# Kernel optimization log

Measured on AMD Instinct MI355X. Metric: run time of the kernel, lower is better.

## Reference

```python
import jax, jax.numpy as jnp
import numpy as np

N = 14           # num_wires
DEPTH = 2        # feature_map_depth; circuit applies DEPTH+1 StronglyEntanglingLayers blocks
SEL_LAYERS = 2   # params (B, 2*N*3) -> weights (B, 2, N, 3)


def _apply_1q(psi, U, w):
    # psi: (B, 2**N) complex64, U: (B,2,2) complex64, acts on wire w (wire 0 = MSB)
    B = psi.shape[0]
    psi = psi.reshape(B, 2 ** w, 2, -1)
    psi = jnp.einsum('bij,bajc->baic', U, psi)
    return psi.reshape(B, -1)


def _apply_cnot(psi, c, t):
    B = psi.shape[0]
    x = psi.reshape((B,) + (2,) * N)
    ca, ta = 1 + c, 1 + t
    a0 = jax.lax.index_in_dim(x, 0, ca, keepdims=True)
    a1 = jnp.flip(jax.lax.index_in_dim(x, 1, ca, keepdims=True), axis=ta)
    return jnp.concatenate([a0, a1], axis=ca).reshape(B, -1)


def _expz(psi, w):
    # <Z_w> = P(bit_w = 0) - P(bit_w = 1)
    B = psi.shape[0]
    p = (psi.real ** 2 + psi.imag ** 2).reshape(B, 2 ** w, 2, -1)
    return p[:, :, 0].sum(axis=(1, 2)) - p[:, :, 1].sum(axis=(1, 2))


def _rot(phi, theta, omega):
    # PennyLane Rot = RZ(omega) RY(theta) RZ(phi); returns (B,2,2) complex
    c, s = jnp.cos(theta / 2), jnp.sin(theta / 2)
    u00 = jnp.exp(-0.5j * (phi + omega)) * c
    u01 = -jnp.exp(0.5j * (phi - omega)) * s
    u10 = jnp.exp(-0.5j * (phi - omega)) * s
    u11 = jnp.exp(0.5j * (phi + omega)) * c
    return jnp.stack([jnp.stack([u00, u01], -1), jnp.stack([u10, u11], -1)], -2)


def _circuit(phases, weights):
    # phases: (B, N) float32, weights: (B, SEL_LAYERS, N, 3) float32
    B = phases.shape[0]
    psi = jnp.zeros((B, 2 ** N), jnp.complex64).at[:, 0].set(1.0)
    # AngleEmbedding (rotation='X'): RX(phi_w) on each wire
    for w in range(N):
        th = phases[:, w] / 2
        c, s = jnp.cos(th), jnp.sin(th)
        U = jnp.stack([jnp.stack([c + 0j, -1j * s], -1),
                       jnp.stack([-1j * s, c + 0j], -1)], -2)
        psi = _apply_1q(psi, U.astype(jnp.complex64), w)
    # (feature_map_depth + 1) StronglyEntanglingLayers blocks, all sharing `weights`
    for _ in range(DEPTH + 1):
        for l in range(SEL_LAYERS):
            for w in range(N):
                U = _rot(weights[:, l, w, 0], weights[:, l, w, 1], weights[:, l, w, 2])
                psi = _apply_1q(psi, U.astype(jnp.complex64), w)
            r = (l % (N - 1)) + 1  # PennyLane default ranges
            for w in range(N):
                psi = _apply_cnot(psi, w, (w + r) % N)
    return jnp.stack([_expz(psi, w) for w in range(N)], axis=1)  # (B, N)


def setup_inputs() -> dict:
    key = jax.random.key(0)
    k1, k2, k3, k4 = jax.random.split(key, 4)
    B = 512
    return {
        'state_batch': jax.random.normal(k1, (B, 2 ** N, 2), jnp.float32),
        'params': jax.random.normal(k2, (B, SEL_LAYERS * N * 3), jnp.float32),
        'head_w': jax.random.normal(k3, (1, N), jnp.float32) / np.float32(np.sqrt(N)),
        'head_b': jax.random.normal(k4, (1,), jnp.float32),
    }


def reference(state_batch, params, head_w, head_b):
    B = state_batch.shape[0]
    # torch.angle of a real tensor: pi where negative, 0 otherwise
    phases = jnp.where(state_batch.reshape(B, -1) < 0,
                       jnp.float32(np.pi), jnp.float32(0.0))[:, :N]
    weights = params.reshape(B, SEL_LAYERS, N, 3)
    qmeas = _circuit(phases, weights)            # (B, N)
    return (qmeas @ head_w.T + head_b)[:, 0]     # (B,)
```

## Files before the change

### kernel.cpp

```cpp
#include <hip/hip_runtime.h>


#define NW 14
#define NSTATE (1 << NW)
#define NTHREADS 1024

typedef float v2f __attribute__((ext_vector_type(2)));
__device__ __forceinline__ v2f spl(float x) { return (v2f){x, x}; }
#define PKF(a, b, c) __builtin_elementwise_fma((a), (b), (c))

__device__ __forceinline__ int SLOT(int i) {
    return i ^ ((((i >> 4) ^ (i >> 7)) & 7) << 1);
}

__device__ __forceinline__ float2 cmul(float2 a, float2 b) {
    return make_float2(a.x * b.x - a.y * b.y, a.x * b.y + a.y * b.x);
}

struct RingConsts { unsigned col[2][NW]; unsigned flow[2][16]; };
constexpr RingConsts make_rc() {
    RingConsts rc{};
    for (int ri = 0; ri < 2; ++ri) {
        for (int bb = 0; bb < NW; ++bb) {
            unsigned x = 1u << bb;
            for (int w = 0; w < NW; ++w) {
                int pc = 13 - w, pt = 13 - ((w + ri + 1) % NW);
                x ^= ((x >> pc) & 1u) << pt;
            }
            rc.col[ri][bb] = x;
        }
        for (int k = 0; k < 16; ++k) {
            unsigned x = 0;
            for (int b = 0; b < 4; ++b) if ((k >> b) & 1) x ^= rc.col[ri][b];
            rc.flow[ri][k] = x;
        }
    }
    return rc;
}
constexpr RingConsts RC = make_rc();

#define LOADUW(w_) \
    const float4 uA = *(const float4*)&R[w_][0]; \
    const float4 uB = *(const float4*)&R[w_][2]; \
    const float u00x = uA.x, u00y = uA.y, u01x = uA.z, u01y = uA.w; \
    const float u10x = uB.x, u10y = uB.y, u11x = uB.z, u11y = uB.w;

#define CBF_CROSS(R0, I0, R1, I1) { \
    const v2f t0r = R0, t0i = I0, t1r = R1, t1i = I1; \
    const v2f X0 = spl(u00x), Y0 = spl(u00y), X1 = spl(u01x), Y1 = spl(u01y); \
    const v2f X2 = spl(u10x), Y2 = spl(u10y), X3 = spl(u11x), Y3 = spl(u11y); \
    R0 = PKF(t0r, X0, PKF(t0i, -Y0, PKF(t1r, X1, t1i * (-Y1)))); \
    I0 = PKF(t0r, Y0, PKF(t0i,  X0, PKF(t1r, Y1, t1i *   X1 ))); \
    R1 = PKF(t0r, X2, PKF(t0i, -Y2, PKF(t1r, X3, t1i * (-Y3)))); \
    I1 = PKF(t0r, Y2, PKF(t0i,  X2, PKF(t1r, Y3, t1i *   X3 ))); }

#define CBF_INTRA(Rr, Ii) { \
    const v2f rl = __builtin_shufflevector(Rr, Rr, 0, 0), rh = __builtin_shufflevector(Rr, Rr, 1, 1); \
    const v2f il = __builtin_shufflevector(Ii, Ii, 0, 0), ih = __builtin_shufflevector(Ii, Ii, 1, 1); \
    const v2f Px0 = (v2f){u00x, u10x}, Px1 = (v2f){u01x, u11x}; \
    const v2f Py0 = (v2f){u00y, u10y}, Py1 = (v2f){u01y, u11y}; \
    Rr = PKF(rl, Px0, PKF(rh, Px1, PKF(il, -Py0, ih * (-Py1)))); \
    Ii = PKF(rl, Py0, PKF(rh, Py1, PKF(il,  Px0, ih *   Px1 ))); }

template<int LO>
__device__ __forceinline__ void rot_pass(float2* st_, const float2 (*R)[4], int t)
{
    const int lowmask = (1 << LO) - 1;
    const int base = ((t >> LO) << (LO + 4)) | (t & lowmask);
#define LD2(j) \
    const float2 eA##j = st_[SLOT(base | ((2*j) << LO))]; \
    const float2 eB##j = st_[SLOT(base | ((2*j+1) << LO))]; \
    v2f RE##j = (v2f){eA##j.x, eB##j.x}, IM##j = (v2f){eA##j.y, eB##j.y};
    LD2(0) LD2(1) LD2(2) LD2(3) LD2(4) LD2(5) LD2(6) LD2(7)
#undef LD2
    {   LOADUW(10 - LO)
        CBF_CROSS(RE0, IM0, RE4, IM4) CBF_CROSS(RE1, IM1, RE5, IM5)
        CBF_CROSS(RE2, IM2, RE6, IM6) CBF_CROSS(RE3, IM3, RE7, IM7) }
    {   LOADUW(11 - LO)
        CBF_CROSS(RE0, IM0, RE2, IM2) CBF_CROSS(RE1, IM1, RE3, IM3)
        CBF_CROSS(RE4, IM4, RE6, IM6) CBF_CROSS(RE5, IM5, RE7, IM7) }
    {   LOADUW(12 - LO)
        CBF_CROSS(RE0, IM0, RE1, IM1) CBF_CROSS(RE2, IM2, RE3, IM3)
        CBF_CROSS(RE4, IM4, RE5, IM5) CBF_CROSS(RE6, IM6, RE7, IM7) }
    {   LOADUW(13 - LO)
        CBF_INTRA(RE0, IM0) CBF_INTRA(RE1, IM1) CBF_INTRA(RE2, IM2) CBF_INTRA(RE3, IM3)
        CBF_INTRA(RE4, IM4) CBF_INTRA(RE5, IM5) CBF_INTRA(RE6, IM6) CBF_INTRA(RE7, IM7) }
#define ST2(j) \
    st_[SLOT(base | ((2*j) << LO))]   = make_float2(RE##j.x, IM##j.x); \
    st_[SLOT(base | ((2*j+1) << LO))] = make_float2(RE##j.y, IM##j.y);
    ST2(0) ST2(1) ST2(2) ST2(3) ST2(4) ST2(5) ST2(6) ST2(7)
#undef ST2
}

#define LOW_LOAD_AND_GATES \
    const int c = (t & 7) ^ ((t >> 3) & 7); \
    const float4* lp = (const float4*)(st_ + (t << 4)); \
    float4 v0 = lp[0 ^ c], v1 = lp[1 ^ c], v2 = lp[2 ^ c], v3 = lp[3 ^ c], \
           v4 = lp[4 ^ c], v5 = lp[5 ^ c], v6 = lp[6 ^ c], v7 = lp[7 ^ c]; \
    v2f RE0 = (v2f){v0.x, v0.z}, IM0 = (v2f){v0.y, v0.w}; \
    v2f RE1 = (v2f){v1.x, v1.z}, IM1 = (v2f){v1.y, v1.w}; \
    v2f RE2 = (v2f){v2.x, v2.z}, IM2 = (v2f){v2.y, v2.w}; \
    v2f RE3 = (v2f){v3.x, v3.z}, IM3 = (v2f){v3.y, v3.w}; \
    v2f RE4 = (v2f){v4.x, v4.z}, IM4 = (v2f){v4.y, v4.w}; \
    v2f RE5 = (v2f){v5.x, v5.z}, IM5 = (v2f){v5.y, v5.w}; \
    v2f RE6 = (v2f){v6.x, v6.z}, IM6 = (v2f){v6.y, v6.w}; \
    v2f RE7 = (v2f){v7.x, v7.z}, IM7 = (v2f){v7.y, v7.w}; \
    {   LOADUW(12)   \
        CBF_CROSS(RE0, IM0, RE1, IM1) CBF_CROSS(RE2, IM2, RE3, IM3) \
        CBF_CROSS(RE4, IM4, RE5, IM5) CBF_CROSS(RE6, IM6, RE7, IM7) } \
    {   LOADUW(13)   \
        CBF_INTRA(RE0, IM0) CBF_INTRA(RE1, IM1) CBF_INTRA(RE2, IM2) CBF_INTRA(RE3, IM3) \
        CBF_INTRA(RE4, IM4) CBF_INTRA(RE5, IM5) CBF_INTRA(RE6, IM6) CBF_INTRA(RE7, IM7) }

__device__ __forceinline__ void rot_low_ring(float2* st_, const float2 (*R)[4], int t,
                                             const unsigned* colr, const unsigned* flowr)
{
    LOW_LOAD_AND_GATES
    unsigned fb = 0;
#pragma unroll
    for (int bit = 4; bit < 14; ++bit)
        if ((t >> (bit - 4)) & 1) fb ^= colr[bit];
    __syncthreads();
#define SC2(j) \
    st_[SLOT((int)(fb ^ flowr[2*j]))]   = make_float2(RE##j.x, IM##j.x); \
    st_[SLOT((int)(fb ^ flowr[2*j+1]))] = make_float2(RE##j.y, IM##j.y);
    SC2(0) SC2(1) SC2(2) SC2(3) SC2(4) SC2(5) SC2(6) SC2(7)
#undef SC2
}

__device__ __forceinline__ float rot_low_meas(float2* st_, const float2 (*R)[4], int t,
                                              const float* s_hw)
{
    LOW_LOAD_AND_GATES
    unsigned fb = 0;
#pragma unroll
    for (int bit = 4; bit < 14; ++bit)
        if ((t >> (bit - 4)) & 1) fb ^= RC.col[1][bit];
#define SGV(b) ((((fb >> b) & 1u) ? -1.f : 1.f) * s_hw[13 - (b)])
    const float sg0 = SGV(0),  sg1 = SGV(1),  sg2 = SGV(2),  sg3 = SGV(3),
                sg4 = SGV(4),  sg5 = SGV(5),  sg6 = SGV(6),  sg7 = SGV(7),
                sg8 = SGV(8),  sg9 = SGV(9),  sg10 = SGV(10), sg11 = SGV(11),
                sg12 = SGV(12), sg13 = SGV(13);
#undef SGV
    const float chiS = ((sg0 + sg1) + (sg2 + sg3)) + ((sg4 + sg5) + (sg6 + sg7))
                     + ((sg8 + sg9) + (sg10 + sg11)) + (sg12 + sg13);
#define SUBSUM(F) ( ((F)&1u?sg0:0.f) + ((F)&2u?sg1:0.f) + ((F)&4u?sg2:0.f) + ((F)&8u?sg3:0.f) \
                  + ((F)&16u?sg4:0.f) + ((F)&32u?sg5:0.f) + ((F)&64u?sg6:0.f) + ((F)&128u?sg7:0.f) \
                  + ((F)&256u?sg8:0.f) + ((F)&512u?sg9:0.f) + ((F)&1024u?sg10:0.f) + ((F)&2048u?sg11:0.f) \
                  + ((F)&4096u?sg12:0.f) + ((F)&8192u?sg13:0.f) )
    v2f acc2 = (v2f){0.f, 0.f};
#define MEAS(j) { \
    const v2f p = PKF(RE##j, RE##j, IM##j * IM##j); \
    const v2f wv = (v2f){ chiS - 2.f * SUBSUM(RC.flow[1][2*j]), \
                          chiS - 2.f * SUBSUM(RC.flow[1][2*j+1]) }; \
    acc2 = PKF(p, wv, acc2); }
    MEAS(0) MEAS(1) MEAS(2) MEAS(3) MEAS(4) MEAS(5) MEAS(6) MEAS(7)
#undef MEAS
#undef SUBSUM
    return acc2.x + acc2.y;
}

__global__ __launch_bounds__(NTHREADS)
__attribute__((amdgpu_waves_per_eu(4, 4)))
void qsim(const float* __restrict__ sb, const float* __restrict__ pr,
          const float* __restrict__ hw, const float* __restrict__ hb,
          float* __restrict__ out)
{
    __shared__ __align__(16) float2 st[NSTATE];
    __shared__ __align__(16) float2 rot[2][NW][4];
    __shared__ unsigned colm[2][NW];
    __shared__ unsigned flow[2][16];
    __shared__ float s_hw[NW];
    __shared__ float s_red[NTHREADS / 64];
    __shared__ unsigned s_bmask;

    const int bid = blockIdx.x;
    const int t = threadIdx.x;

    if (t < 28) {
        int l = t / NW, w = t % NW;
        const float* p = pr + bid * 84 + l * 42 + w * 3;
        float phi = p[0], th = p[1], om = p[2];
        float s, cth;  __sincosf(0.5f * th, &s, &cth);
        float sa, ca, sd, cd;
        __sincosf(0.5f * (phi + om), &sa, &ca);
        __sincosf(0.5f * (phi - om), &sd, &cd);
        rot[l][w][0] = make_float2(ca * cth, -sa * cth);
        rot[l][w][1] = make_float2(-cd * s, -sd * s);
        rot[l][w][2] = make_float2(cd * s, -sd * s);
        rot[l][w][3] = make_float2(ca * cth, sa * cth);
    }
    if (t >= 64 && t < 92) {
        int j = t - 64, ri = j / NW, bb = j % NW;
        colm[ri][bb] = RC.col[ri][bb];
    }
    if (t >= 96 && t < 128) {
        int j = t - 96;
        flow[j >> 4][j & 15] = RC.flow[j >> 4][j & 15];
    }
    if (t >= 128 && t < 142) s_hw[t - 128] = hw[t - 128];
    if (t == 192) {
        const float* row = sb + (size_t)bid * (NSTATE * 2);
        unsigned m = 0;
        for (int w = 0; w < NW; ++w) m |= (row[w] < 0.0f ? 1u : 0u) << (13 - w);
        s_bmask = m;
    }
    __syncthreads();

    {
        const unsigned bm = s_bmask;
        float2 ph = make_float2(1.f, 0.f);
#pragma unroll
        for (int w = 0; w < 10; ++w) {
            int v = (t >> (9 - w)) & 1;
            int bw = (bm >> (13 - w)) & 1;
            ph = cmul(ph, rot[0][w][v * 2 + bw]);
        }
        unsigned fb = 0;
#pragma unroll
        for (int bit = 4; bit < 14; ++bit)
            if ((t >> (bit - 4)) & 1) fb ^= RC.col[0][bit];
#pragma unroll
        for (int k = 0; k < 16; ++k) {
            float2 pl = rot[0][10][(((k >> 3) & 1) * 2) + ((bm >> 3) & 1)];
            pl = cmul(pl, rot[0][11][(((k >> 2) & 1) * 2) + ((bm >> 2) & 1)]);
            pl = cmul(pl, rot[0][12][(((k >> 1) & 1) * 2) + ((bm >> 1) & 1)]);
            pl = cmul(pl, rot[0][13][((k & 1) * 2) + (bm & 1)]);
            st[SLOT((int)(fb ^ RC.flow[0][k]))] = cmul(ph, pl);
        }
    }
    __syncthreads();

#pragma unroll 1
    for (int rep = 0; rep < 4; ++rep) {
        const int l = (rep & 1) ? 0 : 1;
        rot_pass<10>(st, rot[l], t); __syncthreads();
        rot_pass<6>(st, rot[l], t);  __syncthreads();
        rot_pass<2>(st, rot[l], t);  __syncthreads();
        rot_low_ring(st, rot[l], t, colm[l], flow[l]);
        __syncthreads();
    }
    rot_pass<10>(st, rot[1], t); __syncthreads();
    rot_pass<6>(st, rot[1], t);  __syncthreads();
    rot_pass<2>(st, rot[1], t);  __syncthreads();
    float acc = rot_low_meas(st, rot[1], t, s_hw);

    for (int off = 32; off > 0; off >>= 1) acc += __shfl_down(acc, off);
    if ((t & 63) == 0) s_red[t >> 6] = acc;
    __syncthreads();
    if (t == 0) {
        float tot = 0.f;
#pragma unroll
        for (int i = 0; i < NTHREADS / 64; ++i) tot += s_red[i];
        out[bid] = tot + hb[0];
    }
}

extern "C" void kernel_launch(void* const* d_in, const int* in_sizes, int n_in,
                              void* d_out, int out_size, void* d_ws, size_t ws_size,
                              hipStream_t stream)
{
    const float* sb = (const float*)d_in[0];
    const float* pr = (const float*)d_in[1];
    const float* hw = (const float*)d_in[2];
    const float* hb = (const float*)d_in[3];
    float* out = (float*)d_out;
    const int B = in_sizes[1] / 84;
    qsim<<<B, NTHREADS, 0, stream>>>(sb, pr, hw, hb, out);
}
```

Before: 209.5 us.

## Switch state to padded LDS layout with packed-FMA complex butterflies and LUT indices

Replaces the XOR-swizzled shared-memory state layout with a padded layout (2 extra slots every 64 entries) and keeps amplitudes as interleaved complex pairs instead of split real/imag vectors. Complex 2x2 gate application now uses inline-asm v_pk_fma/v_pk_mul with op_sel broadcasting, using precomputed gate coefficient layouts. The per-thread ring permutation base is computed from two small shared lookup tables instead of a 10-step XOR loop. This aims to cut ALU shuffle work and bank conflicts, at the cost of slightly more LDS and hand-written asm that the compiler cannot schedule around.

```diff
diff --git a/kernel.cpp b/kernel.cpp
--- a/kernel.cpp
+++ b/kernel.cpp
@@ -4,17 +4,33 @@
 #define NW 14
 #define NSTATE (1 << NW)
 #define NTHREADS 1024
+#define STATE_SLOTS (NSTATE + ((NSTATE >> 6) << 1))
+
+__device__ __forceinline__ int SLOT(int i) { return i + ((i >> 6) << 1); }
 
 typedef float v2f __attribute__((ext_vector_type(2)));
-__device__ __forceinline__ v2f spl(float x) { return (v2f){x, x}; }
-#define PKF(a, b, c) __builtin_elementwise_fma((a), (b), (c))
-
-__device__ __forceinline__ int SLOT(int i) {
-    return i ^ ((((i >> 4) ^ (i >> 7)) & 7) << 1);
-}
 
 __device__ __forceinline__ float2 cmul(float2 a, float2 b) {
     return make_float2(a.x * b.x - a.y * b.y, a.x * b.y + a.y * b.x);
+}
+
+__device__ __forceinline__ v2f pk_mul_bl(v2f a, v2f b) {
+    v2f d;
+    asm("v_pk_mul_f32 %0, %1, %2 op_sel:[0,0] op_sel_hi:[1,0]"
+        : "=v"(d) : "v"(a), "v"(b));
+    return d;
+}
+__device__ __forceinline__ v2f pk_fma_bl(v2f a, v2f b, v2f c) {
+    v2f d;
+    asm("v_pk_fma_f32 %0, %1, %2, %3 op_sel:[0,0,0] op_sel_hi:[1,0,1]"
+        : "=v"(d) : "v"(a), "v"(b), "v"(c));
+    return d;
+}
+__device__ __forceinline__ v2f pk_fma_sw(v2f a, v2f b, v2f c) {
+    v2f d;
+    asm("v_pk_fma_f32 %0, %1, %2, %3 op_sel:[1,0,0] op_sel_hi:[0,1,1]"
+        : "=v"(d) : "v"(a), "v"(b), "v"(c));
+    return d;
 }
 
 struct RingConsts { unsigned col[2][NW]; unsigned flow[2][16]; };
@@ -39,103 +55,98 @@
 }
 constexpr RingConsts RC = make_rc();
 
-#define LOADUW(w_) \
-    const float4 uA = *(const float4*)&R[w_][0]; \
-    const float4 uB = *(const float4*)&R[w_][2]; \
-    const float u00x = uA.x, u00y = uA.y, u01x = uA.z, u01y = uA.w; \
-    const float u10x = uB.x, u10y = uB.y, u11x = uB.z, u11y = uB.w;
-
-#define CBF_CROSS(R0, I0, R1, I1) { \
-    const v2f t0r = R0, t0i = I0, t1r = R1, t1i = I1; \
-    const v2f X0 = spl(u00x), Y0 = spl(u00y), X1 = spl(u01x), Y1 = spl(u01y); \
-    const v2f X2 = spl(u10x), Y2 = spl(u10y), X3 = spl(u11x), Y3 = spl(u11y); \
-    R0 = PKF(t0r, X0, PKF(t0i, -Y0, PKF(t1r, X1, t1i * (-Y1)))); \
-    I0 = PKF(t0r, Y0, PKF(t0i,  X0, PKF(t1r, Y1, t1i *   X1 ))); \
-    R1 = PKF(t0r, X2, PKF(t0i, -Y2, PKF(t1r, X3, t1i * (-Y3)))); \
-    I1 = PKF(t0r, Y2, PKF(t0i,  X2, PKF(t1r, Y3, t1i *   X3 ))); }
-
-#define CBF_INTRA(Rr, Ii) { \
-    const v2f rl = __builtin_shufflevector(Rr, Rr, 0, 0), rh = __builtin_shufflevector(Rr, Rr, 1, 1); \
-    const v2f il = __builtin_shufflevector(Ii, Ii, 0, 0), ih = __builtin_shufflevector(Ii, Ii, 1, 1); \
-    const v2f Px0 = (v2f){u00x, u10x}, Px1 = (v2f){u01x, u11x}; \
-    const v2f Py0 = (v2f){u00y, u10y}, Py1 = (v2f){u01y, u11y}; \
-    Rr = PKF(rl, Px0, PKF(rh, Px1, PKF(il, -Py0, ih * (-Py1)))); \
-    Ii = PKF(rl, Py0, PKF(rh, Py1, PKF(il,  Px0, ih *   Px1 ))); }
+#define GSTAGE(W) \
+    const float4 g0 = G4[(W)*4+0], g1 = G4[(W)*4+1], \
+                 g2 = G4[(W)*4+2], g3 = G4[(W)*4+3]; \
+    const v2f U00 = (v2f){g0.x,g0.y}, V00 = (v2f){g0.z,g0.w}; \
+    const v2f U01 = (v2f){g1.x,g1.y}, V01 = (v2f){g1.z,g1.w}; \
+    const v2f U10 = (v2f){g2.x,g2.y}, V10 = (v2f){g2.z,g2.w}; \
+    const v2f U11 = (v2f){g3.x,g3.y}, V11 = (v2f){g3.z,g3.w};
+
+#define CBFA(X, Y) { \
+    v2f n0 = pk_mul_bl(X, U00); n0 = pk_fma_sw(X, V00, n0); \
+    n0 = pk_fma_bl(Y, U01, n0); n0 = pk_fma_sw(Y, V01, n0); \
+    v2f n1 = pk_mul_bl(X, U10); n1 = pk_fma_sw(X, V10, n1); \
+    n1 = pk_fma_bl(Y, U11, n1); n1 = pk_fma_sw(Y, V11, n1); \
+    X = n0; Y = n1; }
 
 template<int LO>
-__device__ __forceinline__ void rot_pass(float2* st_, const float2 (*R)[4], int t)
-{
+__device__ __forceinline__ void rot_pass(float2* st_, const float4* G4, int t)
+{
+    constexpr int S = (1 << LO) + ((LO >= 6) ? (1 << (LO - 5)) : 0);
     const int lowmask = (1 << LO) - 1;
     const int base = ((t >> LO) << (LO + 4)) | (t & lowmask);
-#define LD2(j) \
-    const float2 eA##j = st_[SLOT(base | ((2*j) << LO))]; \
-    const float2 eB##j = st_[SLOT(base | ((2*j+1) << LO))]; \
-    v2f RE##j = (v2f){eA##j.x, eB##j.x}, IM##j = (v2f){eA##j.y, eB##j.y};
-    LD2(0) LD2(1) LD2(2) LD2(3) LD2(4) LD2(5) LD2(6) LD2(7)
-#undef LD2
-    {   LOADUW(10 - LO)
-        CBF_CROSS(RE0, IM0, RE4, IM4) CBF_CROSS(RE1, IM1, RE5, IM5)
-        CBF_CROSS(RE2, IM2, RE6, IM6) CBF_CROSS(RE3, IM3, RE7, IM7) }
-    {   LOADUW(11 - LO)
-        CBF_CROSS(RE0, IM0, RE2, IM2) CBF_CROSS(RE1, IM1, RE3, IM3)
-        CBF_CROSS(RE4, IM4, RE6, IM6) CBF_CROSS(RE5, IM5, RE7, IM7) }
-    {   LOADUW(12 - LO)
-        CBF_CROSS(RE0, IM0, RE1, IM1) CBF_CROSS(RE2, IM2, RE3, IM3)
-        CBF_CROSS(RE4, IM4, RE5, IM5) CBF_CROSS(RE6, IM6, RE7, IM7) }
-    {   LOADUW(13 - LO)
-        CBF_INTRA(RE0, IM0) CBF_INTRA(RE1, IM1) CBF_INTRA(RE2, IM2) CBF_INTRA(RE3, IM3)
-        CBF_INTRA(RE4, IM4) CBF_INTRA(RE5, IM5) CBF_INTRA(RE6, IM6) CBF_INTRA(RE7, IM7) }
-#define ST2(j) \
-    st_[SLOT(base | ((2*j) << LO))]   = make_float2(RE##j.x, IM##j.x); \
-    st_[SLOT(base | ((2*j+1) << LO))] = make_float2(RE##j.y, IM##j.y);
-    ST2(0) ST2(1) ST2(2) ST2(3) ST2(4) ST2(5) ST2(6) ST2(7)
-#undef ST2
-}
-
-#define LOW_LOAD_AND_GATES \
-    const int c = (t & 7) ^ ((t >> 3) & 7); \
-    const float4* lp = (const float4*)(st_ + (t << 4)); \
-    float4 v0 = lp[0 ^ c], v1 = lp[1 ^ c], v2 = lp[2 ^ c], v3 = lp[3 ^ c], \
-           v4 = lp[4 ^ c], v5 = lp[5 ^ c], v6 = lp[6 ^ c], v7 = lp[7 ^ c]; \
-    v2f RE0 = (v2f){v0.x, v0.z}, IM0 = (v2f){v0.y, v0.w}; \
-    v2f RE1 = (v2f){v1.x, v1.z}, IM1 = (v2f){v1.y, v1.w}; \
-    v2f RE2 = (v2f){v2.x, v2.z}, IM2 = (v2f){v2.y, v2.w}; \
-    v2f RE3 = (v2f){v3.x, v3.z}, IM3 = (v2f){v3.y, v3.w}; \
-    v2f RE4 = (v2f){v4.x, v4.z}, IM4 = (v2f){v4.y, v4.w}; \
-    v2f RE5 = (v2f){v5.x, v5.z}, IM5 = (v2f){v5.y, v5.w}; \
-    v2f RE6 = (v2f){v6.x, v6.z}, IM6 = (v2f){v6.y, v6.w}; \
-    v2f RE7 = (v2f){v7.x, v7.z}, IM7 = (v2f){v7.y, v7.w}; \
-    {   LOADUW(12)   \
-        CBF_CROSS(RE0, IM0, RE1, IM1) CBF_CROSS(RE2, IM2, RE3, IM3) \
-        CBF_CROSS(RE4, IM4, RE5, IM5) CBF_CROSS(RE6, IM6, RE7, IM7) } \
-    {   LOADUW(13)   \
-        CBF_INTRA(RE0, IM0) CBF_INTRA(RE1, IM1) CBF_INTRA(RE2, IM2) CBF_INTRA(RE3, IM3) \
-        CBF_INTRA(RE4, IM4) CBF_INTRA(RE5, IM5) CBF_INTRA(RE6, IM6) CBF_INTRA(RE7, IM7) }
-
-__device__ __forceinline__ void rot_low_ring(float2* st_, const float2 (*R)[4], int t,
-                                             const unsigned* colr, const unsigned* flowr)
-{
-    LOW_LOAD_AND_GATES
-    unsigned fb = 0;
-#pragma unroll
-    for (int bit = 4; bit < 14; ++bit)
-        if ((t >> (bit - 4)) & 1) fb ^= colr[bit];
-    __syncthreads();
-#define SC2(j) \
-    st_[SLOT((int)(fb ^ flowr[2*j]))]   = make_float2(RE##j.x, IM##j.x); \
-    st_[SLOT((int)(fb ^ flowr[2*j+1]))] = make_float2(RE##j.y, IM##j.y);
-    SC2(0) SC2(1) SC2(2) SC2(3) SC2(4) SC2(5) SC2(6) SC2(7)
-#undef SC2
-}
-
-__device__ __forceinline__ float rot_low_meas(float2* st_, const float2 (*R)[4], int t,
+    float2* p = st_ + SLOT(base);
+    float2* q = p + 8 * S;
+    v2f A0  = *(const v2f*)(p + 0*S), A1  = *(const v2f*)(p + 1*S),
+        A2  = *(const v2f*)(p + 2*S), A3  = *(const v2f*)(p + 3*S),
+        A4  = *(const v2f*)(p + 4*S), A5  = *(const v2f*)(p + 5*S),
+        A6  = *(const v2f*)(p + 6*S), A7  = *(const v2f*)(p + 7*S),
+        A8  = *(const v2f*)(q + 0*S), A9  = *(const v2f*)(q + 1*S),
+        A10 = *(const v2f*)(q + 2*S), A11 = *(const v2f*)(q + 3*S),
+        A12 = *(const v2f*)(q + 4*S), A13 = *(const v2f*)(q + 5*S),
+        A14 = *(const v2f*)(q + 6*S), A15 = *(const v2f*)(q + 7*S);
+    { GSTAGE(13 - LO - 3)
+      CBFA(A0,A8) CBFA(A1,A9) CBFA(A2,A10) CBFA(A3,A11)
+      CBFA(A4,A12) CBFA(A5,A13) CBFA(A6,A14) CBFA(A7,A15) }
+    { GSTAGE(13 - LO - 2)
+      CBFA(A0,A4) CBFA(A1,A5) CBFA(A2,A6) CBFA(A3,A7)
+      CBFA(A8,A12) CBFA(A9,A13) CBFA(A10,A14) CBFA(A11,A15) }
+    { GSTAGE(13 - LO - 1)
+      CBFA(A0,A2) CBFA(A1,A3) CBFA(A4,A6) CBFA(A5,A7)
+      CBFA(A8,A10) CBFA(A9,A11) CBFA(A12,A14) CBFA(A13,A15) }
+    { GSTAGE(13 - LO)
+      CBFA(A0,A1) CBFA(A2,A3) CBFA(A4,A5) CBFA(A6,A7)
+      CBFA(A8,A9) CBFA(A10,A11) CBFA(A12,A13) CBFA(A14,A15) }
+    *(v2f*)(p + 0*S) = A0;  *(v2f*)(p + 1*S) = A1;
+    *(v2f*)(p + 2*S) = A2;  *(v2f*)(p + 3*S) = A3;
+    *(v2f*)(p + 4*S) = A4;  *(v2f*)(p + 5*S) = A5;
+    *(v2f*)(p + 6*S) = A6;  *(v2f*)(p + 7*S) = A7;
+    *(v2f*)(q + 0*S) = A8;  *(v2f*)(q + 1*S) = A9;
+    *(v2f*)(q + 2*S) = A10; *(v2f*)(q + 3*S) = A11;
+    *(v2f*)(q + 4*S) = A12; *(v2f*)(q + 5*S) = A13;
+    *(v2f*)(q + 6*S) = A14; *(v2f*)(q + 7*S) = A15;
+}
+
+#define LOW_LOAD_GATES \
+    float2* pc = st_ + SLOT(t << 4); \
+    const float4* lp = (const float4*)pc; \
+    const float4 r0 = lp[0], r1 = lp[1], r2 = lp[2], r3 = lp[3], \
+                 r4 = lp[4], r5 = lp[5], r6 = lp[6], r7 = lp[7]; \
+    v2f A0  = (v2f){r0.x,r0.y}, A1  = (v2f){r0.z,r0.w}, \
+        A2  = (v2f){r1.x,r1.y}, A3  = (v2f){r1.z,r1.w}, \
+        A4  = (v2f){r2.x,r2.y}, A5  = (v2f){r2.z,r2.w}, \
+        A6  = (v2f){r3.x,r3.y}, A7  = (v2f){r3.z,r3.w}, \
+        A8  = (v2f){r4.x,r4.y}, A9  = (v2f){r4.z,r4.w}, \
+        A10 = (v2f){r5.x,r5.y}, A11 = (v2f){r5.z,r5.w}, \
+        A12 = (v2f){r6.x,r6.y}, A13 = (v2f){r6.z,r6.w}, \
+        A14 = (v2f){r7.x,r7.y}, A15 = (v2f){r7.z,r7.w}; \
+    { GSTAGE(12) \
+      CBFA(A0,A2) CBFA(A1,A3) CBFA(A4,A6) CBFA(A5,A7) \
+      CBFA(A8,A10) CBFA(A9,A11) CBFA(A12,A14) CBFA(A13,A15) } \
+    { GSTAGE(13) \
+      CBFA(A0,A1) CBFA(A2,A3) CBFA(A4,A5) CBFA(A6,A7) \
+      CBFA(A8,A9) CBFA(A10,A11) CBFA(A12,A13) CBFA(A14,A15) }
+
+template<int RI>
+__device__ __forceinline__ void rot_low_ring(float2* st_, const float4* G4, int t,
+                                             const unsigned* lutA_, const unsigned* lutB_)
+{
+    LOW_LOAD_GATES
+    const unsigned fb = lutA_[t & 31] ^ lutB_[t >> 5];
+    __syncthreads();
+#define SCT(k, Ak) st_[SLOT((int)(fb ^ RC.flow[RI][k]))] = make_float2(Ak.x, Ak.y);
+    SCT(0,A0) SCT(1,A1) SCT(2,A2) SCT(3,A3) SCT(4,A4) SCT(5,A5) SCT(6,A6) SCT(7,A7)
+    SCT(8,A8) SCT(9,A9) SCT(10,A10) SCT(11,A11) SCT(12,A12) SCT(13,A13) SCT(14,A14) SCT(15,A15)
+#undef SCT
+}
+
+__device__ __forceinline__ float rot_low_meas(float2* st_, const float4* G4, int t,
+                                              const unsigned* lutA_, const unsigned* lutB_,
                                               const float* s_hw)
 {
-    LOW_LOAD_AND_GATES
-    unsigned fb = 0;
-#pragma unroll
-    for (int bit = 4; bit < 14; ++bit)
-        if ((t >> (bit - 4)) & 1) fb ^= RC.col[1][bit];
+    LOW_LOAD_GATES
+    const unsigned fb = lutA_[t & 31] ^ lutB_[t >> 5];
 #define SGV(b) ((((fb >> b) & 1u) ? -1.f : 1.f) * s_hw[13 - (b)])
     const float sg0 = SGV(0),  sg1 = SGV(1),  sg2 = SGV(2),  sg3 = SGV(3),
                 sg4 = SGV(4),  sg5 = SGV(5),  sg6 = SGV(6),  sg7 = SGV(7),
@@ -148,16 +159,16 @@
                   + ((F)&16u?sg4:0.f) + ((F)&32u?sg5:0.f) + ((F)&64u?sg6:0.f) + ((F)&128u?sg7:0.f) \
                   + ((F)&256u?sg8:0.f) + ((F)&512u?sg9:0.f) + ((F)&1024u?sg10:0.f) + ((F)&2048u?sg11:0.f) \
                   + ((F)&4096u?sg12:0.f) + ((F)&8192u?sg13:0.f) )
-    v2f acc2 = (v2f){0.f, 0.f};
-#define MEAS(j) { \
-    const v2f p = PKF(RE##j, RE##j, IM##j * IM##j); \
-    const v2f wv = (v2f){ chiS - 2.f * SUBSUM(RC.flow[1][2*j]), \
-                          chiS - 2.f * SUBSUM(RC.flow[1][2*j+1]) }; \
-    acc2 = PKF(p, wv, acc2); }
-    MEAS(0) MEAS(1) MEAS(2) MEAS(3) MEAS(4) MEAS(5) MEAS(6) MEAS(7)
-#undef MEAS
+    float acc = 0.f;
+#define MEASA(k, Ak) { const float p2 = fmaf(Ak.x, Ak.x, Ak.y * Ak.y); \
+    acc = fmaf(p2, chiS - 2.f * SUBSUM(RC.flow[1][k]), acc); }
+    MEASA(0,A0) MEASA(1,A1) MEASA(2,A2) MEASA(3,A3)
+    MEASA(4,A4) MEASA(5,A5) MEASA(6,A6) MEASA(7,A7)
+    MEASA(8,A8) MEASA(9,A9) MEASA(10,A10) MEASA(11,A11)
+    MEASA(12,A12) MEASA(13,A13) MEASA(14,A14) MEASA(15,A15)
+#undef MEASA
 #undef SUBSUM
-    return acc2.x + acc2.y;
+    return acc;
 }
 
 __global__ __launch_bounds__(NTHREADS)
@@ -166,10 +177,9 @@
           const float* __restrict__ hw, const float* __restrict__ hb,
           float* __restrict__ out)
 {
-    __shared__ __align__(16) float2 st[NSTATE];
-    __shared__ __align__(16) float2 rot[2][NW][4];
-    __shared__ unsigned colm[2][NW];
-    __shared__ unsigned flow[2][16];
+    __shared__ __align__(16) float2 st[STATE_SLOTS];
+    __shared__ __align__(16) float4 rotc[2][NW * 4];
+    __shared__ unsigned lutA[2][32], lutB[2][32];
     __shared__ float s_hw[NW];
     __shared__ float s_red[NTHREADS / 64];
     __shared__ unsigned s_bmask;
@@ -185,21 +195,24 @@
         float sa, ca, sd, cd;
         __sincosf(0.5f * (phi + om), &sa, &ca);
         __sincosf(0.5f * (phi - om), &sd, &cd);
-        rot[l][w][0] = make_float2(ca * cth, -sa * cth);
-        rot[l][w][1] = make_float2(-cd * s, -sd * s);
-        rot[l][w][2] = make_float2(cd * s, -sd * s);
-        rot[l][w][3] = make_float2(ca * cth, sa * cth);
-    }
-    if (t >= 64 && t < 92) {
-        int j = t - 64, ri = j / NW, bb = j % NW;
-        colm[ri][bb] = RC.col[ri][bb];
-    }
-    if (t >= 96 && t < 128) {
-        int j = t - 96;
-        flow[j >> 4][j & 15] = RC.flow[j >> 4][j & 15];
-    }
-    if (t >= 128 && t < 142) s_hw[t - 128] = hw[t - 128];
-    if (t == 192) {
+        const float u00x = ca * cth, u00y = -sa * cth;
+        const float u01x = -cd * s,  u01y = -sd * s;
+        const float u10x = cd * s,   u10y = -sd * s;
+        const float u11x = ca * cth, u11y = sa * cth;
+        rotc[l][w*4+0] = make_float4(u00x, u00y, -u00y, u00y);
+        rotc[l][w*4+1] = make_float4(u01x, u01y, -u01y, u01y);
+        rotc[l][w*4+2] = make_float4(u10x, u10y, -u10y, u10y);
+        rotc[l][w*4+3] = make_float4(u11x, u11y, -u11y, u11y);
+    }
+    if (t >= 64 && t < 192) {
+        int j = t - 64, ri = j >> 6, tb = (j >> 5) & 1, m = j & 31;
+        unsigned x = 0;
+        for (int b = 0; b < 5; ++b)
+            if ((m >> b) & 1) x ^= RC.col[ri][(tb ? 9 : 4) + b];
+        if (tb) lutB[ri][m] = x; else lutA[ri][m] = x;
+    }
+    if (t >= 192 && t < 206) s_hw[t - 192] = hw[t - 192];
+    if (t == 224) {
         const float* row = sb + (size_t)bid * (NSTATE * 2);
         unsigned m = 0;
         for (int w = 0; w < NW; ++w) m |= (row[w] < 0.0f ? 1u : 0u) << (13 - w);
@@ -214,18 +227,18 @@
         for (int w = 0; w < 10; ++w) {
             int v = (t >> (9 - w)) & 1;
             int bw = (bm >> (13 - w)) & 1;
-            ph = cmul(ph, rot[0][w][v * 2 + bw]);
-        }
-        unsigned fb = 0;
-#pragma unroll
-        for (int bit = 4; bit < 14; ++bit)
-            if ((t >> (bit - 4)) & 1) fb ^= RC.col[0][bit];
+            float4 e = rotc[0][w*4 + v*2 + bw];
+            ph = cmul(ph, make_float2(e.x, e.y));
+        }
+        const unsigned fb = lutA[0][t & 31] ^ lutB[0][t >> 5];
 #pragma unroll
         for (int k = 0; k < 16; ++k) {
-            float2 pl = rot[0][10][(((k >> 3) & 1) * 2) + ((bm >> 3) & 1)];
-            pl = cmul(pl, rot[0][11][(((k >> 2) & 1) * 2) + ((bm >> 2) & 1)]);
-            pl = cmul(pl, rot[0][12][(((k >> 1) & 1) * 2) + ((bm >> 1) & 1)]);
-            pl = cmul(pl, rot[0][13][((k & 1) * 2) + (bm & 1)]);
+            float4 e3 = rotc[0][10*4 + (((k >> 3) & 1) * 2) + ((bm >> 3) & 1)];
+            float4 e2 = rotc[0][11*4 + (((k >> 2) & 1) * 2) + ((bm >> 2) & 1)];
+            float4 e1 = rotc[0][12*4 + (((k >> 1) & 1) * 2) + ((bm >> 1) & 1)];
+            float4 e0 = rotc[0][13*4 + ((k & 1) * 2) + (bm & 1)];
+            float2 pl = cmul(cmul(make_float2(e3.x, e3.y), make_float2(e2.x, e2.y)),
+                             cmul(make_float2(e1.x, e1.y), make_float2(e0.x, e0.y)));
             st[SLOT((int)(fb ^ RC.flow[0][k]))] = cmul(ph, pl);
         }
     }
@@ -234,16 +247,18 @@
 #pragma unroll 1
     for (int rep = 0; rep < 4; ++rep) {
         const int l = (rep & 1) ? 0 : 1;
-        rot_pass<10>(st, rot[l], t); __syncthreads();
-        rot_pass<6>(st, rot[l], t);  __syncthreads();
-        rot_pass<2>(st, rot[l], t);  __syncthreads();
-        rot_low_ring(st, rot[l], t, colm[l], flow[l]);
+        const float4* G4 = &rotc[l][0];
+        rot_pass<10>(st, G4, t); __syncthreads();
+        rot_pass<6>(st, G4, t);  __syncthreads();
+        rot_pass<2>(st, G4, t);  __syncthreads();
+        if (l) rot_low_ring<1>(st, G4, t, lutA[1], lutB[1]);
+        else   rot_low_ring<0>(st, G4, t, lutA[0], lutB[0]);
         __syncthreads();
     }
-    rot_pass<10>(st, rot[1], t); __syncthreads();
-    rot_pass<6>(st, rot[1], t);  __syncthreads();
-    rot_pass<2>(st, rot[1], t);  __syncthreads();
-    float acc = rot_low_meas(st, rot[1], t, s_hw);
+    rot_pass<10>(st, &rotc[1][0], t); __syncthreads();
+    rot_pass<6>(st, &rotc[1][0], t); __syncthreads();
+    rot_pass<2>(st, &rotc[1][0], t); __syncthreads();
+    float acc = rot_low_meas(st, &rotc[1][0], t, lutA[1], lutB[1], s_hw);
 
     for (int off = 32; off > 0; off >>= 1) acc += __shfl_down(acc, off);
     if ((t & 63) == 0) s_red[t >> 6] = acc;
```

Result: no change. 208.9 us (-0.3%).
